# Kernel tuning notes

Hardware: AMD Instinct MI355X
Metric: run time of the kernel (lower is better)

The kernel has to match this reference:

```python
import jax, jax.numpy as jnp
import numpy as np

N = 100000   # nodes
E = 1600000  # directed edges (avg degree 16)
H = 64       # MODEL_HIDDEN_CHANNELS


def setup_inputs() -> dict:
    key = jax.random.key(0)
    ks = jax.random.split(key, 6)
    x = jax.random.normal(ks[0], (N, 1), dtype=jnp.float32)
    edge_index = jax.random.randint(ks[1], (2, E), 0, N, dtype=jnp.int32)
    w1 = jax.random.normal(ks[2], (1, H), dtype=jnp.float32) * 0.5
    b1 = jnp.zeros((H,), dtype=jnp.float32)
    w2 = jax.random.normal(ks[3], (H, H), dtype=jnp.float32) * (1.0 / np.sqrt(H))
    b2 = jnp.zeros((H,), dtype=jnp.float32)
    wfc = jax.random.normal(ks[4], (H, 1), dtype=jnp.float32) * (1.0 / np.sqrt(H))
    bfc = jnp.zeros((1,), dtype=jnp.float32)
    return {"x": x, "edge_index": edge_index, "w1": w1, "b1": b1,
            "w2": w2, "b2": b2, "wfc": wfc, "bfc": bfc}


def _gcn_conv(x, src, dst, norm, W, b, n):
    # PyG GCNConv: h = x @ W, then scatter-add of norm-weighted messages at dst, + bias
    h = x @ W                                   # [n, out]
    msg = h[src] * norm[:, None]                # gather + scale, [e, out]
    agg = jax.ops.segment_sum(msg, dst, num_segments=n)
    return agg + b


def reference(x, edge_index, w1, b1, w2, b2, wfc, bfc):
    n = x.shape[0]
    # add self-loops (PyG GCNConv default)
    loops = jnp.arange(n, dtype=edge_index.dtype)
    src = jnp.concatenate([edge_index[0], loops])
    dst = jnp.concatenate([edge_index[1], loops])
    # symmetric degree normalization D^{-1/2} A_hat D^{-1/2}
    deg = jax.ops.segment_sum(jnp.ones(src.shape[0], dtype=x.dtype), dst, num_segments=n)
    dinv = jnp.where(deg > 0, jax.lax.rsqrt(deg), 0.0)
    norm = dinv[src] * dinv[dst]
    h = jax.nn.relu(_gcn_conv(x, src, dst, norm, w1, b1, n))
    h = jax.nn.relu(_gcn_conv(h, src, dst, norm, w2, b2, n))
    out = h @ wfc + bfc                         # [n, 1]
    return out.reshape(-1)
```

## Files before the change

kernel.cpp:

```cpp
#include <hip/hip_runtime.h>


#define HCH 64
#define CHUNK 4096
#define BSH 7
#define BSZ 128
#define NBMAX 1024

__device__ __forceinline__ void lds_addf(float* p, float v) {
    __hip_atomic_fetch_add(p, v, __ATOMIC_RELAXED, __HIP_MEMORY_SCOPE_WORKGROUP);
}

__global__ __launch_bounds__(512) void k_init(int nb, int cap,
                                              int* __restrict__ cursor,
                                              int* __restrict__ ov_cursor,
                                              const float* __restrict__ w1,
                                              const float* __restrict__ b1,
                                              const float* __restrict__ w2,
                                              float* __restrict__ P) {
    __shared__ float part[8][4][HCH];
    __shared__ float sPo[4 * HCH];
    __shared__ float fsum;
    int t = threadIdx.x;
    for (int i = t; i < nb; i += 512) cursor[i] = i * cap;
    if (t == 0) { *ov_cursor = 0; fsum = 0.f; }
    int j = t & 63, seg = t >> 6;
    float pp = 0.f, pm = 0.f, bp = 0.f, bm = 0.f;
#pragma unroll
    for (int kk = 0; kk < 8; kk++) {
        int k = seg * 8 + kk;
        float w = w1[k], b = b1[k], v = w2[k * HCH + j];
        if (w > 0.f) { pp += w * v; bp += b * v; }
        else if (w < 0.f) { pm += w * v; bm += b * v; }
        else { float rb = b > 0.f ? b : 0.f; bp += rb * v; bm += rb * v; }
    }
    part[seg][0][j] = pp; part[seg][1][j] = pm;
    part[seg][2][j] = bp; part[seg][3][j] = bm;
    __syncthreads();
    if (t < 4 * HCH) {
        int c = t >> 6, jj = t & 63;
        float s = 0.f;
#pragma unroll
        for (int g = 0; g < 8; g++) s += part[g][c][jj];
        sPo[t] = s;
        P[t] = s;
        if (c >= 2) lds_addf(&fsum, fabsf(s));
    }
    __syncthreads();
    if (t == 0) P[4 * HCH] = fsum;
}

__global__ __launch_bounds__(512) void k_place(const int* __restrict__ src,
                                               const int* __restrict__ dst, int e,
                                               int nb, int cap,
                                               int* __restrict__ cursor,
                                               int* __restrict__ ov_cursor,
                                               int* __restrict__ packed,
                                               int2* __restrict__ ovbuf) {
    __shared__ int h[NBMAX];
    __shared__ int basel[NBMAX];
    __shared__ int avail[NBMAX];
    __shared__ int lpv[CHUNK];
    __shared__ short lb[CHUNK];
    int t = threadIdx.x;
    for (int i = t; i < nb; i += 512) h[i] = 0;
    __syncthreads();
    int cbase = blockIdx.x * CHUNK;
    int rem = min(e - cbase, CHUNK);
#pragma unroll
    for (int g = 0; g < 2; g++) {
        int li = t * 8 + g * 4;
        if (li + 3 < rem) {
            int4 s4 = *(const int4*)(src + cbase + li);
            int4 d4 = *(const int4*)(dst + cbase + li);
#pragma unroll
            for (int q = 0; q < 4; q++) {
                int sv = (q == 0) ? s4.x : (q == 1) ? s4.y : (q == 2) ? s4.z : s4.w;
                int dv = (q == 0) ? d4.x : (q == 1) ? d4.y : (q == 2) ? d4.z : d4.w;
                int b = dv >> BSH;
                atomicAdd(&h[b], 1);
                lpv[li + q] = sv | ((dv & (BSZ - 1)) << 17);
                lb[li + q] = (short)b;
            }
        } else {
            for (int q = li; q < rem && q < li + 4; q++) {
                int sv = src[cbase + q], dv = dst[cbase + q];
                int b = dv >> BSH;
                atomicAdd(&h[b], 1);
                lpv[q] = sv | ((dv & (BSZ - 1)) << 17);
                lb[q] = (short)b;
            }
        }
    }
    __syncthreads();
    for (int i = t; i < nb; i += 512) {
        int my = h[i];
        int av = 0, base = 0;
        if (my) {
            base = atomicAdd(&cursor[i], my);
            int room = (i + 1) * cap - base;
            av = room < 0 ? 0 : (room > my ? my : room);
        }
        basel[i] = base;
        avail[i] = av;
        h[i] = 0;
    }
    __syncthreads();
    for (int li = t * 8; li < t * 8 + 8 && li < rem; li++) {
        int b = lb[li];
        int pv = lpv[li];
        int loc = atomicAdd(&h[b], 1);
        if (loc < avail[b]) {
            packed[basel[b] + loc] = pv;
        } else {
            int op = atomicAdd(ov_cursor, 1);
            ovbuf[op] = make_int2(pv & 0x1FFFF, (b << BSH) | (pv >> 17));
        }
    }
}

__global__ __launch_bounds__(512) void k_bdeg(const int* __restrict__ packed,
                                              const int* __restrict__ cursor,
                                              const int* __restrict__ ov_cursor,
                                              const int2* __restrict__ ovbuf,
                                              int cap, const float* __restrict__ x, int n,
                                              float* __restrict__ dinv,
                                              float* __restrict__ y) {
    __shared__ int cnt[BSZ];
    int bk = blockIdx.x, t = threadIdx.x;
    int bbase = bk * cap;
    int bcnt = min(cursor[bk] - bbase, cap);
    if (t < BSZ) cnt[t] = 0;
    __syncthreads();
    for (int base = 0; base < bcnt; base += 2048) {
        int i0 = base + t * 4;
        if (i0 + 3 < bcnt) {
            int4 p = *(const int4*)(packed + bbase + i0);
            atomicAdd(&cnt[p.x >> 17], 1);
            atomicAdd(&cnt[p.y >> 17], 1);
            atomicAdd(&cnt[p.z >> 17], 1);
            atomicAdd(&cnt[p.w >> 17], 1);
        } else {
            for (int i = i0; i < bcnt && i < i0 + 4; i++)
                atomicAdd(&cnt[packed[bbase + i] >> 17], 1);
        }
    }
    int ovc = *ov_cursor;
    for (int i = t; i < ovc; i += 512) {
        int2 o = ovbuf[i];
        if ((o.y >> BSH) == bk) atomicAdd(&cnt[o.y & (BSZ - 1)], 1);
    }
    __syncthreads();
    int node = (bk << BSH) + t;
    if (t < BSZ && node < n) {
        float dv = rsqrtf((float)(cnt[t] + 1));
        dinv[node] = dv;
        y[node] = dv * x[node];
    }
}

__global__ __launch_bounds__(512) void k_bagg1(const int* __restrict__ packed,
                                               const int* __restrict__ cursor,
                                               const int* __restrict__ ov_cursor,
                                               const int2* __restrict__ ovbuf,
                                               int cap, const float* __restrict__ x,
                                               const float* __restrict__ dinv,
                                               const float* __restrict__ y, int n,
                                               float2* __restrict__ val2) {
    __shared__ float acc[BSZ];
    int bk = blockIdx.x, t = threadIdx.x;
    int bbase = bk * cap;
    int bcnt = min(cursor[bk] - bbase, cap);
    if (t < BSZ) acc[t] = 0.f;
    __syncthreads();
    for (int base = 0; base < bcnt; base += 2048) {
        int i0 = base + t * 4;
        if (i0 + 3 < bcnt) {
            int4 p = *(const int4*)(packed + bbase + i0);
            float y0 = y[p.x & 0x1FFFF], y1 = y[p.y & 0x1FFFF];
            float y2 = y[p.z & 0x1FFFF], y3 = y[p.w & 0x1FFFF];
            lds_addf(&acc[p.x >> 17], y0);
            lds_addf(&acc[p.y >> 17], y1);
            lds_addf(&acc[p.z >> 17], y2);
            lds_addf(&acc[p.w >> 17], y3);
        } else {
            for (int i = i0; i < bcnt && i < i0 + 4; i++) {
                int p = packed[bbase + i];
                lds_addf(&acc[p >> 17], y[p & 0x1FFFF]);
            }
        }
    }
    int ovc = *ov_cursor;
    for (int i = t; i < ovc; i += 512) {
        int2 o = ovbuf[i];
        if ((o.y >> BSH) == bk) lds_addf(&acc[o.y & (BSZ - 1)], y[o.x]);
    }
    __syncthreads();
    int node = (bk << BSH) + t;
    if (t < BSZ && node < n) {
        float dv = dinv[node];
        float s = dv * (acc[t] + dv * x[node]);
        val2[node] = make_float2(dv * s, dv);
    }
}

__global__ __launch_bounds__(512) void k_bagg2(const int* __restrict__ packed,
                                               const int* __restrict__ cursor,
                                               const int* __restrict__ ov_cursor,
                                               const int2* __restrict__ ovbuf,
                                               int cap, const float2* __restrict__ val2,
                                               const float* __restrict__ dinv,
                                               const float* __restrict__ P,
                                               const float* __restrict__ b2,
                                               const float* __restrict__ wfc,
                                               const float* __restrict__ bfc,
                                               float* __restrict__ out, int n) {
    __shared__ float aa[2 * BSZ];
    __shared__ float cc[2 * BSZ];
    __shared__ float sP[4 * HCH], sb2[HCH], swfc[HCH];
    __shared__ float sflag;
    int bk = blockIdx.x, t = threadIdx.x;
    int bbase = bk * cap;
    int bcnt = min(cursor[bk] - bbase, cap);
    if (t < 2 * BSZ) { aa[t] = 0.f; cc[t] = 0.f; }
    if (t < 4 * HCH) sP[t] = P[t];
    if (t >= 256 && t < 320) sb2[t - 256] = b2[t - 256];
    if (t >= 320 && t < 384) swfc[t - 320] = wfc[t - 320];
    if (t == 448) sflag = P[4 * HCH];
    __syncthreads();
    bool useB = sflag != 0.f;
    for (int base = 0; base < bcnt; base += 2048) {
        int i0 = base + t * 4;
        if (i0 + 3 < bcnt) {
            int4 p = *(const int4*)(packed + bbase + i0);
            float2 v0 = val2[p.x & 0x1FFFF], v1 = val2[p.y & 0x1FFFF];
            float2 v2 = val2[p.z & 0x1FFFF], v3 = val2[p.w & 0x1FFFF];
            int o0 = (v0.x > 0.f ? 0 : BSZ) + (p.x >> 17);
            int o1 = (v1.x > 0.f ? 0 : BSZ) + (p.y >> 17);
            int o2 = (v2.x > 0.f ? 0 : BSZ) + (p.z >> 17);
            int o3 = (v3.x > 0.f ? 0 : BSZ) + (p.w >> 17);
            lds_addf(&aa[o0], v0.x); lds_addf(&aa[o1], v1.x);
            lds_addf(&aa[o2], v2.x); lds_addf(&aa[o3], v3.x);
            if (useB) {
                lds_addf(&cc[o0], v0.y); lds_addf(&cc[o1], v1.y);
                lds_addf(&cc[o2], v2.y); lds_addf(&cc[o3], v3.y);
            }
        } else {
            for (int i = i0; i < bcnt && i < i0 + 4; i++) {
                int p = packed[bbase + i];
                float2 v = val2[p & 0x1FFFF];
                int off = (v.x > 0.f ? 0 : BSZ) + (p >> 17);
                lds_addf(&aa[off], v.x);
                if (useB) lds_addf(&cc[off], v.y);
            }
        }
    }
    int ovc = *ov_cursor;
    for (int i = t; i < ovc; i += 512) {
        int2 o = ovbuf[i];
        if ((o.y >> BSH) == bk) {
            float2 v = val2[o.x];
            int off = (v.x > 0.f ? 0 : BSZ) + (o.y & (BSZ - 1));
            lds_addf(&aa[off], v.x);
            if (useB) lds_addf(&cc[off], v.y);
        }
    }
    __syncthreads();
    int node = (bk << BSH) + t;
    if (t >= BSZ || node >= n) return;
    float a_p = aa[t], a_m = aa[BSZ + t], c_p = cc[t], c_m = cc[BSZ + t];
    float2 sv = val2[node];
    if (sv.x > 0.f) { a_p += sv.x; c_p += sv.y; }
    else            { a_m += sv.x; c_m += sv.y; }
    float dv = dinv[node];
    float acc = 0.f;
#pragma unroll 8
    for (int j = 0; j < HCH; j++) {
        float z = dv * (a_p * sP[j] + a_m * sP[HCH + j] +
                        c_p * sP[2 * HCH + j] + c_m * sP[3 * HCH + j]) + sb2[j];
        z = z > 0.f ? z : 0.f;
        acc += z * swfc[j];
    }
    out[node] = acc + bfc[0];
}

extern "C" void kernel_launch(void* const* d_in, const int* in_sizes, int n_in,
                              void* d_out, int out_size, void* d_ws, size_t ws_size,
                              hipStream_t stream) {
    const float* x   = (const float*)d_in[0];
    const int*   ei  = (const int*)d_in[1];
    const float* w1  = (const float*)d_in[2];
    const float* b1  = (const float*)d_in[3];
    const float* w2  = (const float*)d_in[4];
    const float* b2  = (const float*)d_in[5];
    const float* wfc = (const float*)d_in[6];
    const float* bfc = (const float*)d_in[7];
    float* out = (float*)d_out;

    const int n = in_sizes[0];
    const int e = in_sizes[1] / 2;
    const int* src = ei;
    const int* dst = ei + e;

    const int nb = (n + BSZ - 1) >> BSH;
    int avg = (e + nb - 1) / nb;
    int cap = ((avg + avg / 4 + 64) + 15) & ~15;

    auto al = [](size_t v) { return (v + 255) & ~(size_t)255; };
    char* ws = (char*)d_ws;
    size_t o = 0;
    int* cursor    = (int*)(ws + o);  o = al(o + (size_t)NBMAX * 4);
    int* ov_cursor = (int*)(ws + o);  o = al(o + 256);
    float* dinv  = (float*)(ws + o);  o = al(o + (size_t)n * 4);
    float* y     = (float*)(ws + o);  o = al(o + (size_t)n * 4);
    float2* val2 = (float2*)(ws + o); o = al(o + (size_t)n * 8);
    float* P     = (float*)(ws + o);  o = al(o + (4 * HCH + 8) * 4);
    int* packed  = (int*)(ws + o);    o = al(o + (size_t)nb * cap * 4);
    int2* ovbuf  = (int2*)(ws + o);   o = al(o + (size_t)e * 8);
    (void)ws_size;

    const int nchunk = (e + CHUNK - 1) / CHUNK;

    k_init<<<1, 512, 0, stream>>>(nb, cap, cursor, ov_cursor, w1, b1, w2, P);
    k_place<<<nchunk, 512, 0, stream>>>(src, dst, e, nb, cap, cursor, ov_cursor,
                                        packed, ovbuf);
    k_bdeg<<<nb, 512, 0, stream>>>(packed, cursor, ov_cursor, ovbuf, cap, x, n, dinv, y);
    k_bagg1<<<nb, 512, 0, stream>>>(packed, cursor, ov_cursor, ovbuf, cap, x, dinv, y,
                                    n, val2);
    k_bagg2<<<nb, 512, 0, stream>>>(packed, cursor, ov_cursor, ovbuf, cap, val2, dinv,
                                    P, b2, wfc, bfc, out, n);
}
```

Measured before the change: 135.1 us.

## Sort edges by bucket in LDS before coalesced scatter in placement kernel

```diff
diff --git a/kernel.cpp b/kernel.cpp
--- a/kernel.cpp
+++ b/kernel.cpp
@@ -2,7 +2,7 @@
 
 
 #define HCH 64
-#define CHUNK 4096
+#define CHUNK 8192
 #define BSH 7
 #define BSZ 128
 #define NBMAX 1024
@@ -19,7 +19,6 @@
                                               const float* __restrict__ w2,
                                               float* __restrict__ P) {
     __shared__ float part[8][4][HCH];
-    __shared__ float sPo[4 * HCH];
     __shared__ float fsum;
     int t = threadIdx.x;
     for (int i = t; i < nb; i += 512) cursor[i] = i * cap;
@@ -42,7 +41,6 @@
         float s = 0.f;
 #pragma unroll
         for (int g = 0; g < 8; g++) s += part[g][c][jj];
-        sPo[t] = s;
         P[t] = s;
         if (c >= 2) lds_addf(&fsum, fabsf(s));
     }
@@ -58,41 +56,35 @@
                                                int* __restrict__ packed,
                                                int2* __restrict__ ovbuf) {
     __shared__ int h[NBMAX];
+    __shared__ int scanE[NBMAX];
     __shared__ int basel[NBMAX];
     __shared__ int avail[NBMAX];
-    __shared__ int lpv[CHUNK];
-    __shared__ short lb[CHUNK];
+    __shared__ int slpv[CHUNK];
+    __shared__ short ssb[CHUNK];
+    __shared__ int wsum[8];
     int t = threadIdx.x;
-    for (int i = t; i < nb; i += 512) h[i] = 0;
+    for (int i = t; i < NBMAX; i += 512) h[i] = 0;
     __syncthreads();
     int cbase = blockIdx.x * CHUNK;
     int rem = min(e - cbase, CHUNK);
-#pragma unroll
-    for (int g = 0; g < 2; g++) {
-        int li = t * 8 + g * 4;
+
+#pragma unroll
+    for (int k = 0; k < CHUNK / 2048; k++) {
+        int li = (k * 512 + t) * 4;
         if (li + 3 < rem) {
-            int4 s4 = *(const int4*)(src + cbase + li);
             int4 d4 = *(const int4*)(dst + cbase + li);
-#pragma unroll
-            for (int q = 0; q < 4; q++) {
-                int sv = (q == 0) ? s4.x : (q == 1) ? s4.y : (q == 2) ? s4.z : s4.w;
-                int dv = (q == 0) ? d4.x : (q == 1) ? d4.y : (q == 2) ? d4.z : d4.w;
-                int b = dv >> BSH;
-                atomicAdd(&h[b], 1);
-                lpv[li + q] = sv | ((dv & (BSZ - 1)) << 17);
-                lb[li + q] = (short)b;
-            }
-        } else {
-            for (int q = li; q < rem && q < li + 4; q++) {
-                int sv = src[cbase + q], dv = dst[cbase + q];
-                int b = dv >> BSH;
-                atomicAdd(&h[b], 1);
-                lpv[q] = sv | ((dv & (BSZ - 1)) << 17);
-                lb[q] = (short)b;
-            }
-        }
-    }
-    __syncthreads();
+            atomicAdd(&h[d4.x >> BSH], 1);
+            atomicAdd(&h[d4.y >> BSH], 1);
+            atomicAdd(&h[d4.z >> BSH], 1);
+            atomicAdd(&h[d4.w >> BSH], 1);
+        } else {
+            for (int q = li; q < rem && q < li + 4; q++)
+                atomicAdd(&h[dst[cbase + q] >> BSH], 1);
+        }
+    }
+    __syncthreads();
+
+    int v0 = h[2 * t], v1 = h[2 * t + 1];
     for (int i = t; i < nb; i += 512) {
         int my = h[i];
         int av = 0, base = 0;
@@ -103,13 +95,65 @@
         }
         basel[i] = base;
         avail[i] = av;
-        h[i] = 0;
-    }
-    __syncthreads();
-    for (int li = t * 8; li < t * 8 + 8 && li < rem; li++) {
-        int b = lb[li];
-        int pv = lpv[li];
-        int loc = atomicAdd(&h[b], 1);
+    }
+    int lane = t & 63, wid = t >> 6;
+    int s = v0 + v1;
+    int incl = s;
+#pragma unroll
+    for (int d = 1; d < 64; d <<= 1) {
+        int o = __shfl_up(incl, d, 64);
+        if (lane >= d) incl += o;
+    }
+    if (lane == 63) wsum[wid] = incl;
+    __syncthreads();
+    if (t < 8) {
+        int v = wsum[t];
+        int inc2 = v;
+#pragma unroll
+        for (int d = 1; d < 8; d <<= 1) {
+            int o = __shfl_up(inc2, d, 8);
+            if (t >= d) inc2 += o;
+        }
+        wsum[t] = inc2 - v;
+    }
+    for (int i = t; i < NBMAX; i += 512) h[i] = 0;
+    __syncthreads();
+    int excl = incl - s + wsum[wid];
+    scanE[2 * t] = excl;
+    scanE[2 * t + 1] = excl + v0;
+    __syncthreads();
+
+#pragma unroll
+    for (int k = 0; k < CHUNK / 2048; k++) {
+        int li = (k * 512 + t) * 4;
+        if (li + 3 < rem) {
+            int4 s4 = *(const int4*)(src + cbase + li);
+            int4 d4 = *(const int4*)(dst + cbase + li);
+#pragma unroll
+            for (int q = 0; q < 4; q++) {
+                int sv = (q == 0) ? s4.x : (q == 1) ? s4.y : (q == 2) ? s4.z : s4.w;
+                int dv = (q == 0) ? d4.x : (q == 1) ? d4.y : (q == 2) ? d4.z : d4.w;
+                int b = dv >> BSH;
+                int pos = scanE[b] + atomicAdd(&h[b], 1);
+                slpv[pos] = sv | ((dv & (BSZ - 1)) << 17);
+                ssb[pos] = (short)b;
+            }
+        } else {
+            for (int q = li; q < rem && q < li + 4; q++) {
+                int sv = src[cbase + q], dv = dst[cbase + q];
+                int b = dv >> BSH;
+                int pos = scanE[b] + atomicAdd(&h[b], 1);
+                slpv[pos] = sv | ((dv & (BSZ - 1)) << 17);
+                ssb[pos] = (short)b;
+            }
+        }
+    }
+    __syncthreads();
+
+    for (int jj = t; jj < rem; jj += 512) {
+        int b = ssb[jj];
+        int loc = jj - scanE[b];
+        int pv = slpv[jj];
         if (loc < avail[b]) {
             packed[basel[b] + loc] = pv;
         } else {
@@ -163,7 +207,7 @@
                                                const int* __restrict__ cursor,
                                                const int* __restrict__ ov_cursor,
                                                const int2* __restrict__ ovbuf,
-                                               int cap, const float* __restrict__ x,
+                                               int cap,
                                                const float* __restrict__ dinv,
                                                const float* __restrict__ y, int n,
                                                float2* __restrict__ val2) {
@@ -199,7 +243,7 @@
     int node = (bk << BSH) + t;
     if (t < BSZ && node < n) {
         float dv = dinv[node];
-        float s = dv * (acc[t] + dv * x[node]);
+        float s = dv * (acc[t] + y[node]);
         val2[node] = make_float2(dv * s, dv);
     }
 }
@@ -325,7 +369,7 @@
     k_place<<<nchunk, 512, 0, stream>>>(src, dst, e, nb, cap, cursor, ov_cursor,
                                         packed, ovbuf);
     k_bdeg<<<nb, 512, 0, stream>>>(packed, cursor, ov_cursor, ovbuf, cap, x, n, dinv, y);
-    k_bagg1<<<nb, 512, 0, stream>>>(packed, cursor, ov_cursor, ovbuf, cap, x, dinv, y,
+    k_bagg1<<<nb, 512, 0, stream>>>(packed, cursor, ov_cursor, ovbuf, cap, dinv, y,
                                     n, val2);
     k_bagg2<<<nb, 512, 0, stream>>>(packed, cursor, ov_cursor, ovbuf, cap, val2, dinv,
                                     P, b2, wfc, bfc, out, n);
```

Result: faster. 129.5 us (-4.2%).
